# Kernel tuning notes

Hardware: AMD Instinct MI355X
Metric: run time of the kernel (lower is better)

Reference implementation:

```python
import jax, jax.numpy as jnp
import numpy as np

LR = 0.01
EPS = 1e-8
D, H, O, N = 1024, 256, 64, 1024


def _normalize(W, b):
    # L2 (Frobenius) normalize weights and biases, clamped at EPS
    wn = jnp.maximum(jnp.sqrt(jnp.sum(W * W)), EPS)
    bn = jnp.maximum(jnp.sqrt(jnp.sum(b * b)), EPS)
    return W / wn, b / bn


def _step(carry, xt):
    W1, b1, W2, b2, W3, b3 = carry
    x, t = xt
    # forward pass (3-layer sigmoid MLP, softmax over -a3 as in original)
    a1 = jax.nn.sigmoid(x @ W1 + b1)
    a2 = jax.nn.sigmoid(a1 @ W2 + b2)
    a3 = jax.nn.sigmoid(a2 @ W3 + b3)
    out = jax.nn.softmax(-a3)
    # manual backprop deltas
    d3 = (t - out) * a3 * (1.0 - a3)
    o2 = (W3 @ d3) * a2 * (1.0 - a2)
    o1 = (W2 @ o2) * a1 * (1.0 - a1)
    # SGD update (note: original subtracts the delta, matching .sub_)
    W3 = W3 - LR * jnp.outer(a2, d3)
    b3 = b3 - LR * d3
    W2 = W2 - LR * jnp.outer(a1, o2)
    b2 = b2 - LR * o2
    W1 = W1 - LR * jnp.outer(x, o1)
    b1 = b1 - LR * o1
    # L2 normalize each layer's weights/biases
    W1, b1 = _normalize(W1, b1)
    W2, b2 = _normalize(W2, b2)
    W3, b3 = _normalize(W3, b3)
    return (W1, b1, W2, b2, W3, b3), None


def setup_inputs() -> dict:
    key = jax.random.key(0)
    k = jax.random.split(key, 5)
    return {
        "training_data": jax.random.normal(k[0], (N, D), jnp.float32),
        "training_targets": jax.random.uniform(k[1], (N, O), dtype=jnp.float32),
        "weights1": jax.random.normal(k[2], (D, H), jnp.float32) * 0.01,
        "biases1": jnp.zeros((H,), jnp.float32),
        "weights2": jax.random.normal(k[3], (H, H), jnp.float32) * 0.01,
        "biases2": jnp.zeros((H,), jnp.float32),
        "weights3": jax.random.normal(k[4], (H, O), jnp.float32) * 0.01,
        "biases3": jnp.zeros((O,), jnp.float32),
    }


def reference(training_data, training_targets, weights1, biases1, weights2, biases2, weights3, biases3):
    carry0 = (weights1, biases1, weights2, biases2, weights3, biases3)
    carry, _ = jax.lax.scan(_step, carry0, (training_data, training_targets))
    W1, b1, W2, b2, W3, b3 = carry
    return (W1, W2, W3)
```

## Files before the change

kernel.cpp:

```cpp
#include <hip/hip_runtime.h>
#include <math.h>


#define LRC  0.01f
#define EPSV 1e-8f

typedef float f32x8 __attribute__((ext_vector_type(8)));

#define SMEM_FLOATS 37768
#define SMEM_BYTES  (SMEM_FLOATS * 4)

#define ROWS16(OP)                                                            \
  OP(0) OP(1) OP(2) OP(3) OP(4) OP(5) OP(6) OP(7)                             \
  OP(8) OP(9) OP(10) OP(11) OP(12) OP(13) OP(14) OP(15)

__device__ __forceinline__ float hsum8(f32x8 v) {
  return ((v.s0 + v.s1) + (v.s2 + v.s3)) + ((v.s4 + v.s5) + (v.s6 + v.s7));
}

template <int CTRL>
__device__ __forceinline__ float dpp_add(float v) {
  const int s = __builtin_amdgcn_update_dpp(0, __builtin_bit_cast(int, v),
                                            CTRL, 0xf, 0xf, true);
  return v + __builtin_bit_cast(float, s);
}

__device__ __forceinline__ float dpp_allred64(float v) {
  v = dpp_add<0x111>(v);
  v = dpp_add<0x112>(v);
  v = dpp_add<0x114>(v);
  v = dpp_add<0x118>(v);
  v = dpp_add<0x142>(v);
  v = dpp_add<0x143>(v);
  return __builtin_bit_cast(float,
      __builtin_amdgcn_readlane(__builtin_bit_cast(int, v), 63));
}

__device__ __forceinline__ float wave_allred(float v) {
#pragma unroll
  for (int off = 32; off > 0; off >>= 1) v += __shfl_xor(v, off);
  return v;
}

__device__ __forceinline__ void wave_fence() {
  __builtin_amdgcn_sched_barrier(0);
  asm volatile("s_waitcnt lgkmcnt(0)" ::: "memory");
  __builtin_amdgcn_sched_barrier(0);
}

__device__ __forceinline__ void lds_spin(volatile int* f, int want) {
  while (*f != want) {}
}

#define FMA16(c, a, b)                                                        \
  c[0][0] += a.x * b.x; c[0][1] += a.x * b.y; c[0][2] += a.x * b.z; c[0][3] += a.x * b.w; \
  c[1][0] += a.y * b.x; c[1][1] += a.y * b.y; c[1][2] += a.y * b.z; c[1][3] += a.y * b.w; \
  c[2][0] += a.z * b.x; c[2][1] += a.z * b.y; c[2][2] += a.z * b.z; c[2][3] += a.z * b.w; \
  c[3][0] += a.w * b.x; c[3][1] += a.w * b.y; c[3][2] += a.w * b.z; c[3][3] += a.w * b.w;

__global__ __launch_bounds__(256) void k_gram(const float* __restrict__ X,
                                              float* __restrict__ G) {
  const int bi = blockIdx.y, bj = blockIdx.x;
  if (bj > bi) return;
  __shared__ float Xa[32][68];
  __shared__ float Xb[32][68];
  const int tid = threadIdx.x;
  const int tx = tid & 15, ty = tid >> 4;
  float c[4][4] = {};
  for (int k0 = 0; k0 < 1024; k0 += 32) {
    __syncthreads();
    {
      const int row = tid >> 2, kk = (tid & 3) * 8;
      const float* pa = X + (bi * 64 + row) * 1024 + k0 + kk;
      const float4 a0 = *(const float4*)pa;
      const float4 a1 = *(const float4*)(pa + 4);
      Xa[kk + 0][row] = a0.x; Xa[kk + 1][row] = a0.y;
      Xa[kk + 2][row] = a0.z; Xa[kk + 3][row] = a0.w;
      Xa[kk + 4][row] = a1.x; Xa[kk + 5][row] = a1.y;
      Xa[kk + 6][row] = a1.z; Xa[kk + 7][row] = a1.w;
      const float* pb = X + (bj * 64 + row) * 1024 + k0 + kk;
      const float4 b0 = *(const float4*)pb;
      const float4 b1 = *(const float4*)(pb + 4);
      Xb[kk + 0][row] = b0.x; Xb[kk + 1][row] = b0.y;
      Xb[kk + 2][row] = b0.z; Xb[kk + 3][row] = b0.w;
      Xb[kk + 4][row] = b1.x; Xb[kk + 5][row] = b1.y;
      Xb[kk + 6][row] = b1.z; Xb[kk + 7][row] = b1.w;
    }
    __syncthreads();
#pragma unroll
    for (int kk = 0; kk < 32; kk++) {
      const float4 a = *(const float4*)&Xa[kk][ty * 4];
      const float4 b = *(const float4*)&Xb[kk][tx * 4];
      FMA16(c, a, b)
    }
  }
#pragma unroll
  for (int ii = 0; ii < 4; ii++) {
    *(float4*)(G + (bi * 64 + ty * 4 + ii) * 1024 + bj * 64 + tx * 4) =
        make_float4(c[ii][0], c[ii][1], c[ii][2], c[ii][3]);
  }
}

__global__ __launch_bounds__(256) void k_z10(const float* __restrict__ X,
                                             const float* __restrict__ W1g,
                                             float* __restrict__ Z10) {
  const int bi = blockIdx.y, bj = blockIdx.x;
  __shared__ float At[32][68];
  __shared__ float Bt[32][68];
  const int tid = threadIdx.x;
  const int tx = tid & 15, ty = tid >> 4;
  float c[4][4] = {};
  for (int k0 = 0; k0 < 1024; k0 += 32) {
    __syncthreads();
    {
      const int row = tid >> 2, kk = (tid & 3) * 8;
      const float* pa = X + (bi * 64 + row) * 1024 + k0 + kk;
      const float4 a0 = *(const float4*)pa;
      const float4 a1 = *(const float4*)(pa + 4);
      At[kk + 0][row] = a0.x; At[kk + 1][row] = a0.y;
      At[kk + 2][row] = a0.z; At[kk + 3][row] = a0.w;
      At[kk + 4][row] = a1.x; At[kk + 5][row] = a1.y;
      At[kk + 6][row] = a1.z; At[kk + 7][row] = a1.w;
      const int kr = tid >> 3, j8 = (tid & 7) * 8;
      const float* pb = W1g + (k0 + kr) * 256 + bj * 64 + j8;
      *(float4*)&Bt[kr][j8]     = *(const float4*)pb;
      *(float4*)&Bt[kr][j8 + 4] = *(const float4*)(pb + 4);
    }
    __syncthreads();
#pragma unroll
    for (int kk = 0; kk < 32; kk++) {
      const float4 a = *(const float4*)&At[kk][ty * 4];
      const float4 b = *(const float4*)&Bt[kk][tx * 4];
      FMA16(c, a, b)
    }
  }
#pragma unroll
  for (int ii = 0; ii < 4; ii++) {
    *(float4*)(Z10 + (bi * 64 + ty * 4 + ii) * 256 + bj * 64 + tx * 4) =
        make_float4(c[ii][0], c[ii][1], c[ii][2], c[ii][3]);
  }
}

__global__ __launch_bounds__(256) void k_w1out(
    const float* __restrict__ X, const float* __restrict__ o1g,
    const float* __restrict__ cg, const float* __restrict__ W1g,
    const float* __restrict__ sclg, float* __restrict__ outW1) {
  const int bi = blockIdx.y, bj = blockIdx.x;
  __shared__ float At[32][68];
  __shared__ float Bt[32][68];
  const int tid = threadIdx.x;
  const int tx = tid & 15, ty = tid >> 4;
  float c[4][4] = {};
  for (int k0 = 0; k0 < 1024; k0 += 32) {
    __syncthreads();
    {
      const int kr = tid >> 3, m8 = (tid & 7) * 8;
      const float* pa = X + (k0 + kr) * 1024 + bi * 64 + m8;
      *(float4*)&At[kr][m8]     = *(const float4*)pa;
      *(float4*)&At[kr][m8 + 4] = *(const float4*)(pa + 4);
      const float cs = cg[k0 + kr];
      const float* pb = o1g + (k0 + kr) * 256 + bj * 64 + m8;
      float4 b0 = *(const float4*)pb;
      float4 b1 = *(const float4*)(pb + 4);
      b0.x *= cs; b0.y *= cs; b0.z *= cs; b0.w *= cs;
      b1.x *= cs; b1.y *= cs; b1.z *= cs; b1.w *= cs;
      *(float4*)&Bt[kr][m8]     = b0;
      *(float4*)&Bt[kr][m8 + 4] = b1;
    }
    __syncthreads();
#pragma unroll
    for (int kk = 0; kk < 32; kk++) {
      const float4 a = *(const float4*)&At[kk][ty * 4];
      const float4 b = *(const float4*)&Bt[kk][tx * 4];
      FMA16(c, a, b)
    }
  }
  const float s1f = sclg[0];
#pragma unroll
  for (int ii = 0; ii < 4; ii++) {
    const int row = bi * 64 + ty * 4 + ii;
    const float4 w = *(const float4*)(W1g + row * 256 + bj * 64 + tx * 4);
    *(float4*)(outW1 + row * 256 + bj * 64 + tx * 4) =
        make_float4(s1f * (w.x + c[ii][0]), s1f * (w.y + c[ii][1]),
                    s1f * (w.z + c[ii][2]), s1f * (w.w + c[ii][3]));
  }
}

__device__ __forceinline__ float block_reduce8(float v, float* tmp, int tid) {
  v = wave_allred(v);
  __syncthreads();
  if ((tid & 63) == 0) tmp[tid >> 6] = v;
  __syncthreads();
  float s = 0.f;
#pragma unroll
  for (int w = 0; w < 8; w++) s += tmp[w];
  __syncthreads();
  return s;
}

#define SUM8(x0, x1) (((x0.x + x0.y) + (x0.z + x0.w)) +                       \
                      ((x1.x + x1.y) + (x1.z + x1.w)))

__global__ __launch_bounds__(512, 1) void k2_seq(
    const float* __restrict__ Tg, const float* __restrict__ W1g,
    const float* __restrict__ b1g, const float* __restrict__ W2g,
    const float* __restrict__ b2g, const float* __restrict__ W3g,
    const float* __restrict__ b3g, const float* __restrict__ G,
    const float* __restrict__ Z10, float* __restrict__ o1g,
    float* __restrict__ cg, float* __restrict__ sclg,
    float* __restrict__ outW2, float* __restrict__ outW3) {
  extern __shared__ float sm[];
  float* const zo   = sm;
  float* const Gb   = sm + 17408;
  float* const scr  = sm + 21504;
  float* const Tb   = sm + 29952;
  float* const a1v  = sm + 34048;
  float* const z1v  = sm + 34560;
  float* const z2v  = sm + 34816;
  float* const a2v  = sm + 35072;
  float* const o2v  = sm + 35328;
  float* const b1ps = sm + 35840;
  float* const b2ps = sm + 36096;
  float* const d3v  = sm + 36352;
  float* const b3ps = sm + 36416;
  float* const ch   = sm + 36480;
  float* const dpart= sm + 36544;
  float* const sca  = sm + 36632;
  float* const cpre = sm + 36644;
  float* const csc  = sm + 36676;
  int*   const flgi = (int*)(sm + 37764);


  const int tid = threadIdx.x;
  const int lane = tid & 63;
  const int w = tid >> 6;
  const int p = tid >> 5;
  const int q = tid & 31;
  const int rown = 32 * w + (lane & 31);

  f32x8 W2_0, W2_1, W2_2, W2_3, W2_4, W2_5, W2_6, W2_7,
        W2_8, W2_9, W2_10, W2_11, W2_12, W2_13, W2_14, W2_15;
  float W3x_0, W3x_1, W3x_2, W3x_3, W3x_4, W3x_5, W3x_6, W3x_7,
        W3x_8, W3x_9, W3x_10, W3x_11, W3x_12, W3x_13, W3x_14, W3x_15;
  float W3y_0, W3y_1, W3y_2, W3y_3, W3y_4, W3y_5, W3y_6, W3y_7,
        W3y_8, W3y_9, W3y_10, W3y_11, W3y_12, W3y_13, W3y_14, W3y_15;

#define INIT_ROW(i)                                                           \
  { const int row = p * 16 + i;                                               \
    W2_##i  = *(const f32x8*)(W2g + row * 256 + q * 8);                       \
    W3x_##i = W3g[row * 64 + q * 2];                                          \
    W3y_##i = W3g[row * 64 + q * 2 + 1]; }
  ROWS16(INIT_ROW)

  if (tid < 256) {
    b1ps[tid] = b1g[tid]; b2ps[tid] = b2g[tid];
    o2v[tid] = 0.f; o2v[256 + tid] = 0.f;
    a1v[tid] = 0.f; a1v[256 + tid] = 0.f;
  }
  if (tid < 64) b3ps[tid] = b3g[tid];
  if (tid == 0) {
    sca[0] = 1.f; sca[1] = 1.f; sca[2] = 1.f; sca[3] = 1.f;
    sca[4] = 1.f; sca[5] = 1.f; sca[6] = 0.f; sca[7] = 0.f;
    sca[8] = -LRC;
    ch[0] = -LRC;
    flgi[0] = -1; flgi[1] = -1; flgi[2] = -1;
  }

  float acc1 = 0.f;
  for (int i = tid; i < 65536; i += 512) {
    const float4 v = ((const float4*)W1g)[i];
    acc1 += v.x * v.x + v.y * v.y + v.z * v.z + v.w * v.w;
  }
  const float n1init = block_reduce8(acc1, scr, tid);
  float acc2 = 0.f;
#define N2_ROW(i) { f32x8 t = W2_##i * W2_##i; acc2 += hsum8(t); }
  ROWS16(N2_ROW)
  const float n2init = block_reduce8(acc2, scr, tid);
  float acc3 = 0.f;
#define N3_ROW(i) acc3 += W3x_##i * W3x_##i + W3y_##i * W3y_##i;
  ROWS16(N3_ROW)
  const float n3init = block_reduce8(acc3, scr, tid);

  float s1 = 1.f, s2 = 1.f, s3 = 1.f;
  float c1cur = -LRC;
  double n1d = (double)n1init;
  float n2 = n2init, n3 = n3init;
  __syncthreads();

  auto chain0 = [&](const int lidx) {
    const float4 qa0 = *(const float4*)&dpart[0];
    const float4 qa1 = *(const float4*)&dpart[4];
    const float4 qb0 = *(const float4*)&dpart[8];
    const float4 qb1 = *(const float4*)&dpart[12];
    const float4 qc0 = *(const float4*)&dpart[16];
    const float4 qc1 = *(const float4*)&dpart[20];
    const float dts0 = SUM8(qa0, qa1);
    const float dts1 = SUM8(qb0, qb1);
    const float dts8 = SUM8(qc0, qc1);
    const double c1d = (double)c1cur;
    const double gtt = (double)Gb[lidx * 65];
    n1d = n1d + 2.0 * c1d * (double)dts0 +
          c1d * c1d * gtt * (double)dts1;
    const double w1n = (double)s1 * sqrt(n1d);
    s1 = (float)((double)s1 / fmax(w1n, (double)EPSV));
    c1cur = -LRC / s1;
    if (lane == 0) {
      if (lidx < 63) ch[lidx + 1] = c1cur;
      sca[0] = s1;
      sca[1] = 1.f / fmaxf(sqrtf(dts8), EPSV);
      sca[8] = c1cur;
    }
  };
  auto chain7 = [&](const int par) {
    const float4 qd0 = *(const float4*)&dpart[24];
    const float4 qd1 = *(const float4*)&dpart[28];
    const float4 qe0 = *(const float4*)&dpart[32];
    const float4 qe1 = *(const float4*)&dpart[36];
    const float4 qf0 = *(const float4*)&dpart[40];
    const float4 qf1 = *(const float4*)&dpart[44];
    const float4 qg0 = *(const float4*)&dpart[48 + par * 8];
    const float4 qg1 = *(const float4*)&dpart[52 + par * 8];
    const float4 qh  = *(const float4*)&dpart[80];
    const float dts2 = SUM8(qd0, qd1);
    const float dts4 = SUM8(qe0, qe1);
    const float dts9 = SUM8(qf0, qf1);
    const float dts3 = SUM8(qg0, qg1);
    const float dts6 = (qh.x + qh.y) + (qh.z + qh.w);
    const float dts5 = dpart[84], dts7 = dpart[85], dts10 = dpart[86];
    const float n2p = n2 - 2.f * LRC * dts2 + LRC * LRC * dts3 * dts4;
    const float r2s = 1.f / fmaxf(sqrtf(n2p), EPSV);
    n2 = n2p * r2s * r2s;
    const float cw2n = -LRC / s2;
    s2 = s2 * r2s;
    const float n3p = n3 - 2.f * LRC * dts5 + LRC * LRC * dts6 * dts7;
    const float r3s = 1.f / fmaxf(sqrtf(n3p), EPSV);
    n3 = n3p * r3s * r3s;
    const float cw3n = -LRC / s3;
    s3 = s3 * r3s;
    if (lane == 0) {
      sca[2] = s2;
      sca[3] = 1.f / fmaxf(sqrtf(dts9), EPSV);
      sca[4] = s3;
      sca[5] = 1.f / fmaxf(sqrtf(dts10), EPSV);
      sca[6] = cw2n;
      sca[7] = cw3n;
    }
  };

  for (int b = 0; b < 16; b++) {
    const int bs = b * 64;
    {
      f32x8 pacc0 = {0.f, 0.f, 0.f, 0.f, 0.f, 0.f, 0.f, 0.f};
      f32x8 pacc1 = pacc0, pacc2 = pacc0, pacc3 = pacc0;
      for (int c0 = 0; c0 < bs; c0 += 32) {
        __syncthreads();
        if (tid < 32) cpre[tid] = cg[c0 + tid];
        {
          const int row = tid >> 3, k4 = (tid & 7) * 4;
          const float4 gv = *(const float4*)(G + (bs + row) * 1024 + c0 + k4);
          Gb[row * 33 + k4 + 0] = gv.x; Gb[row * 33 + k4 + 1] = gv.y;
          Gb[row * 33 + k4 + 2] = gv.z; Gb[row * 33 + k4 + 3] = gv.w;
        }
#pragma unroll
        for (int u = 0; u < 4; u++) {
          const int fi = tid + u * 512;
          ((float4*)scr)[fi] = ((const float4*)(o1g + c0 * 256))[fi];
        }
        __syncthreads();
#pragma unroll 2
        for (int ss = 0; ss < 32; ss++) {
          const float cs = cpre[ss];
          const f32x8 o8 = *(const f32x8*)(scr + ss * 256 + q * 8);
          pacc0 += (Gb[(p * 4 + 0) * 33 + ss] * cs) * o8;
          pacc1 += (Gb[(p * 4 + 1) * 33 + ss] * cs) * o8;
          pacc2 += (Gb[(p * 4 + 2) * 33 + ss] * cs) * o8;
          pacc3 += (Gb[(p * 4 + 3) * 33 + ss] * cs) * o8;
        }
      }
      __syncthreads();
#define ZSTORE(rr)                                                            \
      { const int row = p * 4 + rr;                                           \
        *(f32x8*)(zo + row * 272 + q * 8) =                                   \
            *(const f32x8*)(Z10 + (bs + row) * 256 + q * 8) + pacc##rr; }
      ZSTORE(0) ZSTORE(1) ZSTORE(2) ZSTORE(3)
#pragma unroll
      for (int u = 0; u < 2; u++) {
        const int fi = tid + u * 512;
        const int row = fi >> 4, c4 = fi & 15;
        *(float4*)(Gb + row * 64 + c4 * 4) =
            *(const float4*)(G + (bs + row) * 1024 + bs + c4 * 4);
      }
      ((float4*)Tb)[tid]       = ((const float4*)(Tg + bs * 64))[tid];
      ((float4*)Tb)[tid + 512] = ((const float4*)(Tg + bs * 64))[tid + 512];
      __syncthreads();
    }

    for (int l = 0; l < 64; l++) {
      const int t = bs + l;
      const int cur = (t & 1) * 256, prv = 256 - cur;

#define W2_UPD()                                                              \
      { const float cw2u = sca[6];                                            \
        const f32x8 o8s = cw2u * (*(const f32x8*)&o2v[prv + q * 8]);          \
        const float* apv = &a1v[prv + p * 16];                                \
        W2_0  += apv[0]  * o8s; W2_1  += apv[1]  * o8s;                       \
        W2_2  += apv[2]  * o8s; W2_3  += apv[3]  * o8s;                       \
        W2_4  += apv[4]  * o8s; W2_5  += apv[5]  * o8s;                       \
        W2_6  += apv[6]  * o8s; W2_7  += apv[7]  * o8s;                       \
        W2_8  += apv[8]  * o8s; W2_9  += apv[9]  * o8s;                       \
        W2_10 += apv[10] * o8s; W2_11 += apv[11] * o8s;                       \
        W2_12 += apv[12] * o8s; W2_13 += apv[13] * o8s;                       \
        W2_14 += apv[14] * o8s; W2_15 += apv[15] * o8s; }

      if (l > 0) {
        if (w == 0) {
          __builtin_amdgcn_s_setprio(1);
          chain0(l - 1);
          __builtin_amdgcn_s_setprio(0);
          wave_fence();
          if (lane == 0) *(volatile int*)&flgi[0] = t;
        } else if (w == 7) {
          __builtin_amdgcn_s_setprio(1);
          chain7((t - 1) & 1);
          __builtin_amdgcn_s_setprio(0);
          wave_fence();
          if (lane == 0) *(volatile int*)&flgi[1] = t;
        }
      }
      {
        const int jp = tid >> 2, quarter = tid & 3;
        float ax = 0.f, ay = 0.f;
        for (int lp = quarter; lp < l; lp += 4) {
          const float gcs = ch[lp] * Gb[l * 64 + lp];
          const float2 zr = *(const float2*)&zo[lp * 272 + 2 * jp];
          ax += gcs * zr.x; ay += gcs * zr.y;
        }
        ax = dpp_add<0xB1>(ax); ax = dpp_add<0x4E>(ax);
        ay = dpp_add<0xB1>(ay); ay = dpp_add<0x4E>(ay);
        if (l > 0) {
          if (w != 0) lds_spin((volatile int*)&flgi[0], t);
          if (w != 7) lds_spin((volatile int*)&flgi[1], t);
        }
        asm volatile("" ::: "memory");
        const float s1c = sca[0], rb1c = sca[1];
        const float2 zop = *(const float2*)&zo[l * 272 + 2 * jp];
        const float2 b1q = *(const float2*)&b1ps[2 * jp];
        const float2 ap  = *(const float2*)&a1v[prv + 2 * jp];
        const float z1u0 = zop.x + ax, z1u1 = zop.y + ay;
        const float a1x0 = 1.f / (1.f + expf(-(s1c * z1u0 + rb1c * b1q.x)));
        const float a1x1 = 1.f / (1.f + expf(-(s1c * z1u1 + rb1c * b1q.y)));
        if (quarter == 0) {
          *(float2*)&z1v[2 * jp] = make_float2(z1u0, z1u1);
          *(float2*)&a1v[cur + 2 * jp] = make_float2(a1x0, a1x1);
        }
        const float v3 = dpp_allred64(
            quarter == 0 ? a1x0 * a1x0 + a1x1 * a1x1 : 0.f);
        const float vad = dpp_allred64(
            quarter == 0 ? a1x0 * ap.x + a1x1 * ap.y : 0.f);
        if (lane == 0) {
          dpart[48 + (t & 1) * 8 + w] = v3;
          dpart[64 + w] = vad;
        }
      }
      if (t > 0) {
        const float cw3c = sca[7];
        const float d0s = cw3c * d3v[q * 2], d1s = cw3c * d3v[q * 2 + 1];
#define UPD3_ROW(i)                                                           \
        { const float a2o = a2v[p * 16 + i];                                  \
          W3x_##i += a2o * d0s; W3y_##i += a2o * d1s; }
        ROWS16(UPD3_ROW)
      }
      __syncthreads();

      {
        f32x8 acc = {0.f, 0.f, 0.f, 0.f, 0.f, 0.f, 0.f, 0.f};
#define B1_ROW(i) acc += a1v[cur + p * 16 + i] * W2_##i;
        ROWS16(B1_ROW)
        *(f32x8*)&scr[p * 264 + q * 8] = acc;
      }
      __syncthreads();

      if (tid < 256) {
        const float s2c = sca[2], rb2c = sca[3], cw2c = sca[6];
        float s = 0.f;
#pragma unroll
        for (int pp = 0; pp < 16; pp++) s += scr[pp * 264 + tid];
        const float adot = ((dpart[64] + dpart[65]) + (dpart[66] + dpart[67]))
                         + ((dpart[68] + dpart[69]) + (dpart[70] + dpart[71]));
        const float z2p = s2c * (s + cw2c * adot * o2v[prv + tid]);
        z2v[tid] = z2p;
        const float a2x = 1.f / (1.f + expf(-(z2p + rb2c * b2ps[tid])));
        a2v[tid] = a2x;
        const float v6 = dpp_allred64(a2x * a2x);
        if ((tid & 63) == 0) dpart[80 + (tid >> 6)] = v6;
      } else if (t > 0) {
        W2_UPD()
      }
      __syncthreads();

      {
        float c0a = 0.f, c1a = 0.f;
#define C1_ROW(i)                                                             \
        { const float a2x = a2v[p * 16 + i];                                  \
          c0a += a2x * W3x_##i; c1a += a2x * W3y_##i; }
        ROWS16(C1_ROW)
        csc[(q * 2 + 0) * 17 + p] = c0a;
        csc[(q * 2 + 1) * 17 + p] = c1a;
      }
      __syncthreads();

      {
        if (w == 7) {
          __builtin_amdgcn_s_setprio(1);
          const float s3c = sca[4], rb3c = sca[5];
          float s = 0.f;
#pragma unroll
          for (int pp = 0; pp < 16; pp++) s += csc[lane * 17 + pp];
          const float z3p = s3c * s;
          const float a3 = 1.f / (1.f + expf(-(z3p + rb3c * b3ps[lane])));
          const float e = expf(-a3);
          const float tot = dpp_allred64(e);
          const float outv = e / tot;
          const float d3 = (Tb[l * 64 + lane] - outv) * a3 * (1.f - a3);
          d3v[lane] = d3;
          const float b3n = rb3c * b3ps[lane] - LRC * d3;
          b3ps[lane] = b3n;
          const float v5 = dpp_allred64(z3p * d3);
          const float v7 = dpp_allred64(d3 * d3);
          const float v10 = dpp_allred64(b3n * b3n);
          if (lane == 0) { dpart[84] = v5; dpart[85] = v7; dpart[86] = v10; }
          __builtin_amdgcn_s_setprio(0);
          wave_fence();
          if (lane == 0) *(volatile int*)&flgi[2] = t;
        } else if (w < 4) {
          if (t > 0) { W2_UPD() }
          lds_spin((volatile int*)&flgi[2], t);
        } else {
          lds_spin((volatile int*)&flgi[2], t);
        }
        asm volatile("" ::: "memory");
        const float s3c = sca[4], rb2c = sca[3];
        const float d0 = d3v[q * 2 + 0], d1 = d3v[q * 2 + 1];
#define E1_ROW(i) scr[(p * 16 + i) * 33 + q] = W3x_##i * d0 + W3y_##i * d1;
        ROWS16(E1_ROW)
        wave_fence();
        float s = 0.f;
#pragma unroll
        for (int qq = 0; qq < 32; qq++) s += scr[rown * 33 + qq];
        const float a2x = a2v[rown];
        const float o2x = s3c * s * a2x * (1.f - a2x);
        const float b2n = rb2c * b2ps[rown] - LRC * o2x;
        const bool own = (lane & 32) == 0;
        if (own) { o2v[cur + rown] = o2x; b2ps[rown] = b2n; }
        const float v2 = dpp_allred64(own ? z2v[rown] * o2x : 0.f);
        const float v4 = dpp_allred64(own ? o2x * o2x : 0.f);
        const float v9 = dpp_allred64(own ? b2n * b2n : 0.f);
        if (lane == 0) {
          dpart[24 + w] = v2; dpart[32 + w] = v4; dpart[40 + w] = v9;
        }
      }
      __syncthreads();

      {
        const float s2c = sca[2], rb1c = sca[1];
        const f32x8 ov8 = *(const f32x8*)&o2v[cur + q * 8];
#define F_ROW(i)                                                              \
        { f32x8 tq = W2_##i * ov8; scr[(p * 16 + i) * 33 + q] = hsum8(tq); }
        ROWS16(F_ROW)
        wave_fence();
        float s = 0.f;
#pragma unroll
        for (int qq = 0; qq < 32; qq++) s += scr[rown * 33 + qq];
        const float a1x = a1v[cur + rown];
        const float o1x = s2c * s * a1x * (1.f - a1x);
        const float b1n = rb1c * b1ps[rown] - LRC * o1x;
        const float z1x = z1v[rown];
        const bool own = (lane & 32) == 0;
        if (own) { zo[l * 272 + rown] = o1x; b1ps[rown] = b1n; }
        const float v0 = dpp_allred64(own ? z1x * o1x : 0.f);
        const float v1 = dpp_allred64(own ? o1x * o1x : 0.f);
        const float v8 = dpp_allred64(own ? b1n * b1n : 0.f);
        if (lane == 0) {
          dpart[0 + w] = v0; dpart[8 + w] = v1; dpart[16 + w] = v8;
        }
      }
      __syncthreads();
    }

    if (w == 0) chain0(63);
    else if (w == 7) chain7((bs + 63) & 1);
    __syncthreads();

    {
#pragma unroll
      for (int u = 0; u < 4; u++) {
        const int chunk = tid + u * 512;
        const int row = chunk >> 5, c8 = chunk & 31;
        *(f32x8*)(o1g + (bs + row) * 256 + c8 * 8) =
            *(const f32x8*)(zo + row * 272 + c8 * 8);
      }
      if (tid < 64) cg[bs + tid] = ch[tid];
      if (tid == 0) ch[0] = sca[8];
    }
  }

  {
    const float cw2f = sca[6], cw3f = sca[7];
    const float s2f = sca[2], s3f = sca[4];
    const f32x8 o8s = cw2f * (*(const f32x8*)&o2v[256 + q * 8]);
    const float d0s = cw3f * d3v[q * 2], d1s = cw3f * d3v[q * 2 + 1];
#define FIN_ROW(i)                                                            \
    { const float a1o = a1v[256 + p * 16 + i];                                \
      W2_##i += a1o * o8s;                                                    \
      const float a2o = a2v[p * 16 + i];                                      \
      W3x_##i += a2o * d0s; W3y_##i += a2o * d1s;                             \
      const int row = p * 16 + i;                                             \
      *(f32x8*)(outW2 + row * 256 + q * 8) = s2f * W2_##i;                    \
      outW3[row * 64 + q * 2]     = s3f * W3x_##i;                            \
      outW3[row * 64 + q * 2 + 1] = s3f * W3y_##i; }
    ROWS16(FIN_ROW)
    if (tid == 0) sclg[0] = sca[0];
  }
}

extern "C" void kernel_launch(void* const* d_in, const int* in_sizes, int n_in,
                              void* d_out, int out_size, void* d_ws,
                              size_t ws_size, hipStream_t stream) {
  (void)in_sizes; (void)n_in; (void)out_size; (void)ws_size;
  const float* X   = (const float*)d_in[0];
  const float* Tg  = (const float*)d_in[1];
  const float* W1g = (const float*)d_in[2];
  const float* b1g = (const float*)d_in[3];
  const float* W2g = (const float*)d_in[4];
  const float* b2g = (const float*)d_in[5];
  const float* W3g = (const float*)d_in[6];
  const float* b3g = (const float*)d_in[7];
  float* out = (float*)d_out;
  float* ws  = (float*)d_ws;

  float* G    = ws;
  float* Z10  = G + 1048576;
  float* o1g  = Z10 + 262144;
  float* cg   = o1g + 262144;
  float* sclg = cg + 1024;

  (void)hipFuncSetAttribute((const void*)k2_seq,
                            hipFuncAttributeMaxDynamicSharedMemorySize,
                            SMEM_BYTES);

  k_gram<<<dim3(16, 16), 256, 0, stream>>>(X, G);
  k_z10<<<dim3(4, 16), 256, 0, stream>>>(X, W1g, Z10);
  k2_seq<<<dim3(1), dim3(512), SMEM_BYTES, stream>>>(
      Tg, W1g, b1g, W2g, b2g, W3g, b3g, G, Z10, o1g, cg, sclg,
      out + 262144, out + 327680);
  k_w1out<<<dim3(4, 16), 256, 0, stream>>>(X, o1g, cg, W1g, sclg, out);
}
```

Measured before the change: 8.279 ms.

## Replace per-step block barriers with per-wave LDS flag handoffs

```diff
diff --git a/kernel.cpp b/kernel.cpp
--- a/kernel.cpp
+++ b/kernel.cpp
@@ -7,7 +7,7 @@
 
 typedef float f32x8 __attribute__((ext_vector_type(8)));
 
-#define SMEM_FLOATS 37768
+#define SMEM_FLOATS 37792
 #define SMEM_BYTES  (SMEM_FLOATS * 4)
 
 #define ROWS16(OP)                                                            \
@@ -50,6 +50,10 @@
 
 __device__ __forceinline__ void lds_spin(volatile int* f, int want) {
   while (*f != want) {}
+}
+__device__ __forceinline__ void lds_spin8(volatile int* f, int want) {
+#pragma unroll
+  for (int i = 0; i < 8; i++) { while (f[i] != want) {} }
 }
 
 #define FMA16(c, a, b)                                                        \
@@ -229,6 +233,9 @@
   float* const cpre = sm + 36644;
   float* const csc  = sm + 36676;
   int*   const flgi = (int*)(sm + 37764);
+  int*   const flgB = (int*)(sm + 37767);
+  int*   const flgC = (int*)(sm + 37775);
+  int*   const flgF = (int*)(sm + 37783);
 
 
   const int tid = threadIdx.x;
@@ -264,6 +271,8 @@
     sca[8] = -LRC;
     ch[0] = -LRC;
     flgi[0] = -1; flgi[1] = -1; flgi[2] = -1;
+#pragma unroll
+    for (int i = 0; i < 8; i++) { flgB[i] = -1; flgC[i] = -1; flgF[i] = -1; }
   }
 
   float acc1 = 0.f;
@@ -301,9 +310,15 @@
     const double gtt = (double)Gb[lidx * 65];
     n1d = n1d + 2.0 * c1d * (double)dts0 +
           c1d * c1d * gtt * (double)dts1;
-    const double w1n = (double)s1 * sqrt(n1d);
-    s1 = (float)((double)s1 / fmax(w1n, (double)EPSV));
-    c1cur = -LRC / s1;
+    const double sq = sqrt(n1d);
+    const double w1n = (double)s1 * sq;
+    if (w1n > (double)EPSV) {
+      s1 = (float)(1.0 / sq);
+      c1cur = (float)(-(double)LRC * sq);
+    } else {
+      s1 = (float)((double)s1 / (double)EPSV);
+      c1cur = -LRC / s1;
+    }
     if (lane == 0) {
       if (lidx < 63) ch[lidx + 1] = c1cur;
       sca[0] = s1;
@@ -414,6 +429,8 @@
 
       if (l > 0) {
         if (w == 0) {
+          lds_spin8((volatile int*)flgF, t - 1);
+          asm volatile("" ::: "memory");
           __builtin_amdgcn_s_setprio(1);
           chain0(l - 1);
           __builtin_amdgcn_s_setprio(0);
@@ -470,21 +487,23 @@
           W3x_##i += a2o * d0s; W3y_##i += a2o * d1s; }
         ROWS16(UPD3_ROW)
       }
-      __syncthreads();
-
+      wave_fence();
       {
         f32x8 acc = {0.f, 0.f, 0.f, 0.f, 0.f, 0.f, 0.f, 0.f};
 #define B1_ROW(i) acc += a1v[cur + p * 16 + i] * W2_##i;
         ROWS16(B1_ROW)
-        *(f32x8*)&scr[p * 264 + q * 8] = acc;
-      }
-      __syncthreads();
+        *(f32x8*)&scr[p * 528 + q * 8] = acc;
+      }
+      wave_fence();
+      if (lane == 0) *(volatile int*)&flgB[w] = t;
 
       if (tid < 256) {
+        lds_spin8((volatile int*)flgB, t);
+        asm volatile("" ::: "memory");
         const float s2c = sca[2], rb2c = sca[3], cw2c = sca[6];
         float s = 0.f;
 #pragma unroll
-        for (int pp = 0; pp < 16; pp++) s += scr[pp * 264 + tid];
+        for (int pp = 0; pp < 16; pp++) s += scr[pp * 528 + tid];
         const float adot = ((dpart[64] + dpart[65]) + (dpart[66] + dpart[67]))
                          + ((dpart[68] + dpart[69]) + (dpart[70] + dpart[71]));
         const float z2p = s2c * (s + cw2c * adot * o2v[prv + tid]);
@@ -507,10 +526,13 @@
         csc[(q * 2 + 0) * 17 + p] = c0a;
         csc[(q * 2 + 1) * 17 + p] = c1a;
       }
-      __syncthreads();
+      wave_fence();
+      if (lane == 0) *(volatile int*)&flgC[w] = t;
 
       {
         if (w == 7) {
+          lds_spin8((volatile int*)flgC, t);
+          asm volatile("" ::: "memory");
           __builtin_amdgcn_s_setprio(1);
           const float s3c = sca[4], rb3c = sca[5];
           float s = 0.f;
@@ -584,8 +606,11 @@
           dpart[0 + w] = v0; dpart[8 + w] = v1; dpart[16 + w] = v8;
         }
       }
-      __syncthreads();
-    }
+      wave_fence();
+      if (lane == 0) *(volatile int*)&flgF[w] = t;
+    }
+
+    __syncthreads();
 
     if (w == 0) chain0(63);
     else if (w == 7) chain7((bs + 63) & 1);
```

Result: slower. 9.388 ms (+13.4%).
